# Performance work log

Measured on AMD Instinct MI355X. Metric: run time of the kernel, lower is better.

Reference implementation:

```python
import jax, jax.numpy as jnp
import numpy as np

NUM_QUBITS = 13
NUM_LAYERS = 2


def setup_inputs() -> dict:
    key = jax.random.key(0)
    k1, k2 = jax.random.split(key)
    x = jax.random.normal(k1, (512, 2 ** NUM_QUBITS), dtype=jnp.float32)
    weights = jax.random.normal(k2, (NUM_LAYERS, NUM_QUBITS, 3), dtype=jnp.float32)
    return {"x": x, "weights": weights}


def _rot_matrix(phi, theta, omega):
    # qml.Rot(phi, theta, omega) = RZ(omega) @ RY(theta) @ RZ(phi)
    c = jnp.cos(theta * 0.5).astype(jnp.complex64)
    s = jnp.sin(theta * 0.5).astype(jnp.complex64)
    e_m = jnp.exp((-0.5j) * (phi + omega).astype(jnp.complex64))
    e_p = jnp.exp((0.5j) * (phi + omega).astype(jnp.complex64))
    e_d = jnp.exp((0.5j) * (phi - omega).astype(jnp.complex64))
    e_dc = jnp.exp((-0.5j) * (phi - omega).astype(jnp.complex64))
    row0 = jnp.stack([e_m * c, -e_d * s])
    row1 = jnp.stack([e_dc * s, e_p * c])
    return jnp.stack([row0, row1])  # (2, 2) complex64


def _apply_1q(psi, U, q):
    # psi: (B, 2, 2, ..., 2); contract qubit axis q with 2x2 gate U
    ax = 1 + q
    psi = jnp.moveaxis(psi, ax, -1)
    psi = psi @ U.T
    return jnp.moveaxis(psi, -1, ax)


def _apply_cnot(psi, c, t):
    # X on target where control bit == 1
    s0 = jax.lax.index_in_dim(psi, 0, axis=1 + c, keepdims=True)
    s1 = jax.lax.index_in_dim(psi, 1, axis=1 + c, keepdims=True)
    s1 = jnp.flip(s1, axis=1 + t)
    return jnp.concatenate([s0, s1], axis=1 + c)


def reference(x, weights):
    n = NUM_QUBITS
    B = x.shape[0]
    # AmplitudeEmbedding with normalize=True
    norm = jnp.sqrt(jnp.sum(x * x, axis=1, keepdims=True))
    psi = (x / norm).astype(jnp.complex64).reshape((B,) + (2,) * n)
    # StronglyEntanglingLayers (default ranges r_l = (l % (n-1)) + 1, CNOT imprimitive)
    for l in range(NUM_LAYERS):
        r = (l % (n - 1)) + 1
        for q in range(n):
            U = _rot_matrix(weights[l, q, 0], weights[l, q, 1], weights[l, q, 2])
            psi = _apply_1q(psi, U, q)
        for q in range(n):
            psi = _apply_cnot(psi, q, (q + r) % n)
    # expval(PauliZ(n // 2)) = p(bit=0) - p(bit=1)
    m = n // 2
    probs = jnp.real(psi) ** 2 + jnp.imag(psi) ** 2
    axes = tuple(i for i in range(1, n + 1) if i != 1 + m)
    p = probs.sum(axis=axes)  # (B, 2)
    return p[:, 0] - p[:, 1]
```

## Files before the change

kernel.cpp:

```cpp
#include <hip/hip_runtime.h>
#include <math.h>

#define NQ    13
#define DIM   8192
#define BLOCK 512
#define NGATE 26


__device__ __forceinline__ int SW(int a) { return a ^ (((a >> 7) & 7) << 2); }

struct PCols { int c[NQ]; };
constexpr PCols make_cols(int r) {
    PCols P{};
    for (int b = 0; b < NQ; ++b) {
        int cc = 1 << b;
        for (int cq = 0; cq < NQ; ++cq) {
            const int cb = 12 - cq;
            const int tb = 12 - ((cq + r) % NQ);
            cc ^= ((cc >> cb) & 1) << tb;
        }
        P.c[b] = cc;
    }
    return P;
}
constexpr PCols C1 = make_cols(1);
constexpr int make_rm6() {
    int m = 0;
    for (int b = 0; b < NQ; ++b) m |= ((make_cols(2).c[b] >> 6) & 1) << b;
    return m;
}
constexpr int RM6 = make_rm6();

struct Combos { int k[16]; };
constexpr Combos make_combos() {
    Combos K{};
    for (int j = 0; j < 16; ++j)
        K.k[j] = ((j & 1) ? C1.c[0] : 0) ^ ((j & 2) ? C1.c[1] : 0)
               ^ ((j & 4) ? C1.c[10] : 0) ^ ((j & 8) ? C1.c[11] : 0);
    return K;
}
constexpr Combos KC = make_combos();

constexpr int make_sjw() {
    int wv = 0;
    for (int j = 0; j < 16; ++j) {
        const int jm = (j & 3) | (((j >> 2) & 3) << 10);
        wv |= (__builtin_popcount(jm & RM6) & 1) << j;
    }
    return wv;
}
constexpr int SJW = make_sjw();

__device__ __forceinline__ float2 f2mul(float s, float2 a) {
    return make_float2(s * a.x, s * a.y);
}
__device__ __forceinline__ float2 f2fma(float s, float2 a, float2 b) {
    return make_float2(fmaf(s, a.x, b.x), fmaf(s, a.y, b.y));
}
__device__ __forceinline__ float2 fswap(float2 a) { return make_float2(-a.y, a.x); }

struct G8 { float4 a, b; };
__device__ __forceinline__ G8 ldg8(const float* gm, int gi) {
    G8 g;
    g.a = *(const float4*)&gm[gi * 8];
    g.b = *(const float4*)&gm[gi * 8 + 4];
    return g;
}

template<int P>
__device__ __forceinline__ void rotp(float2* c, const G8 g) {
    #pragma unroll
    for (int m = 0; m < 8; ++m) {
        const int j0 = ((m >> P) << (P + 1)) | (m & ((1 << P) - 1));
        const int j1 = j0 | (1 << P);
        const float2 a0 = c[j0], a1 = c[j1];
        const float2 s0 = fswap(a0), s1 = fswap(a1);
        c[j0] = f2fma(g.a.w, s1, f2fma(g.a.z, a1, f2fma(g.a.y, s0, f2mul(g.a.x, a0))));
        c[j1] = f2fma(g.b.w, s1, f2fma(g.b.z, a1, f2fma(g.b.y, s0, f2mul(g.b.x, a0))));
    }
}

template<int CTRL>
__device__ __forceinline__ float dppx(float v) {
    return __int_as_float(
        __builtin_amdgcn_update_dpp(0, __float_as_int(v), CTRL, 0xf, 0xf, true));
}
template<int CTRL>
__device__ __forceinline__ void rotlane(float2* c, const G8 g, const bool hi) {
    const float Ar = hi ? g.b.z : g.a.x;
    const float Ai = hi ? g.b.w : g.a.y;
    const float Br = hi ? g.b.x : g.a.z;
    const float Bi = hi ? g.b.y : g.a.w;
    #pragma unroll
    for (int j = 0; j < 16; ++j) {
        const float2 p  = make_float2(dppx<CTRL>(c[j].x), dppx<CTRL>(c[j].y));
        const float2 so = fswap(c[j]), sp = fswap(p);
        c[j] = f2fma(Bi, sp, f2fma(Br, p, f2fma(Ai, so, f2mul(Ar, c[j]))));
    }
}

__device__ __forceinline__ void loadgrp(const float* re, const float* im, int a, float2* c) {
    const float4 r = *(const float4*)&re[a];
    const float4 i = *(const float4*)&im[a];
    c[0] = make_float2(r.x, i.x); c[1] = make_float2(r.y, i.y);
    c[2] = make_float2(r.z, i.z); c[3] = make_float2(r.w, i.w);
}
__device__ __forceinline__ void storegrp(float* re, float* im, int a, const float2* c) {
    *(float4*)&re[a] = make_float4(c[0].x, c[1].x, c[2].x, c[3].x);
    *(float4*)&im[a] = make_float4(c[0].y, c[1].y, c[2].y, c[3].y);
}

__global__ __launch_bounds__(BLOCK, 4) void qsim_kernel(
    const float* __restrict__ x,
    const float* __restrict__ w,
    float* __restrict__ out)
{
    __shared__ __align__(16) float re[DIM];
    __shared__ __align__(16) float im[DIM];
    __shared__ __align__(16) float gm[NGATE * 8];
    __shared__ float red_ss[8], red_acc[8];

    const int b = blockIdx.x;
    const int t = threadIdx.x;

    if (t < NGATE) {
        const float phi = w[t * 3 + 0], theta = w[t * 3 + 1], omega = w[t * 3 + 2];
        float co, si;  sincosf(0.5f * theta, &si, &co);
        float sps, cps, sds, cds;
        sincosf(0.5f * (phi + omega), &sps, &cps);
        sincosf(0.5f * (phi - omega), &sds, &cds);
        float* g = &gm[t * 8];
        g[0] =  cps * co;  g[1] = -sps * co;
        g[2] = -cds * si;  g[3] = -sds * si;
        g[4] =  cds * si;  g[5] = -sds * si;
        g[6] =  cps * co;  g[7] =  sps * co;
    }

    const float4* x4 = (const float4*)(x + (size_t)b * DIM);
    float ss = 0.f;
    #pragma unroll
    for (int k = 0; k < 4; ++k) {
        const int m = t + BLOCK * k;
        const int a = SW(4 * m);
        const float4 v = x4[m];
        *(float4*)&re[a] = v;
        ss += v.x * v.x + v.y * v.y + v.z * v.z + v.w * v.w;
    }
    #pragma unroll
    for (int off = 32; off > 0; off >>= 1) ss += __shfl_down(ss, off, 64);
    if ((t & 63) == 0) red_ss[t >> 6] = ss;
    __syncthreads();
    float total = 0.f;
    #pragma unroll
    for (int i = 0; i < 8; ++i) total += red_ss[i];

    float2 c[16];

    const int base2 = (((t >> 2) & 15) << 2) | ((t & 3) << 8) | (((t >> 6) & 7) << 10);
    const int base3 = (((t >> 1) & 255) << 2) | ((t & 1) << 12);

    #pragma unroll
    for (int l = 0; l < 2; ++l) {
        const int G = l * 13;

        if (l == 0) {
            #pragma unroll
            for (int g = 0; g < 4; ++g) {
                const float4 r = *(const float4*)&re[SW((t << 4) | (g << 2))];
                c[4 * g + 0] = make_float2(r.x, 0.f);
                c[4 * g + 1] = make_float2(r.y, 0.f);
                c[4 * g + 2] = make_float2(r.z, 0.f);
                c[4 * g + 3] = make_float2(r.w, 0.f);
            }
        } else {
            #pragma unroll
            for (int g = 0; g < 4; ++g)
                loadgrp(re, im, SW((t << 4) | (g << 2)), &c[4 * g]);
        }
        rotp<0>(c, ldg8(gm, G + 12));
        rotp<1>(c, ldg8(gm, G + 11));
        rotp<2>(c, ldg8(gm, G + 10));
        rotp<3>(c, ldg8(gm, G +  9));
        rotlane<0xB1>(c, ldg8(gm, G + 8), (t & 1) != 0);
        rotlane<0x4E>(c, ldg8(gm, G + 7), (t & 2) != 0);
        #pragma unroll
        for (int g = 0; g < 4; ++g)
            storegrp(re, im, SW((t << 4) | (g << 2)), &c[4 * g]);
        __syncthreads();

        #pragma unroll
        for (int h = 0; h < 4; ++h) loadgrp(re, im, SW(base2 | (h << 6)), &c[4 * h]);
        rotp<2>(c, ldg8(gm, G + 6));
        rotp<3>(c, ldg8(gm, G + 5));
        rotlane<0xB1>(c, ldg8(gm, G + 4), (t & 1) != 0);
        rotlane<0x4E>(c, ldg8(gm, G + 3), (t & 2) != 0);
        #pragma unroll
        for (int h = 0; h < 4; ++h) storegrp(re, im, SW(base2 | (h << 6)), &c[4 * h]);
        __syncthreads();

        #pragma unroll
        for (int h = 0; h < 4; ++h) loadgrp(re, im, SW(base3 | (h << 10)), &c[4 * h]);
        if (l == 0) __syncthreads();
        rotp<2>(c, ldg8(gm, G + 2));
        rotp<3>(c, ldg8(gm, G + 1));
        rotlane<0xB1>(c, ldg8(gm, G + 0), (t & 1) != 0);

        if (l == 0) {
            int mb = 0;
            if (t & 1) mb ^= C1.c[12];
            #pragma unroll
            for (int bb = 0; bb < 8; ++bb)
                if ((t >> (bb + 1)) & 1) mb ^= C1.c[2 + bb];
            #pragma unroll
            for (int j = 0; j < 16; ++j) {
                const int a = SW(mb ^ KC.k[j]);
                re[a] = c[j].x; im[a] = c[j].y;
            }
            __syncthreads();
        }
    }

    const int sbase = __popc(base3 & RM6) & 1;
    float acc = 0.f;
    #pragma unroll
    for (int j = 0; j < 16; ++j) {
        const float p = c[j].x * c[j].x + c[j].y * c[j].y;
        acc += (sbase ^ ((SJW >> j) & 1)) ? -p : p;
    }
    #pragma unroll
    for (int off = 32; off > 0; off >>= 1) acc += __shfl_down(acc, off, 64);
    if ((t & 63) == 0) red_acc[t >> 6] = acc;
    __syncthreads();
    if (t == 0) {
        float tot = 0.f;
        #pragma unroll
        for (int i = 0; i < 8; ++i) tot += red_acc[i];
        out[b] = tot / total;
    }
}

extern "C" void kernel_launch(void* const* d_in, const int* in_sizes, int n_in,
                              void* d_out, int out_size, void* d_ws, size_t ws_size,
                              hipStream_t stream) {
    const float* x = (const float*)d_in[0];
    const float* w = (const float*)d_in[1];
    float* out = (float*)d_out;
    const int B = in_sizes[0] / DIM;
    qsim_kernel<<<B, BLOCK, 0, stream>>>(x, w, out);
}
```

Baseline: 85.02 us.

## Process two batch rows per block to amortize gate loads and barriers

Each block now simulates two state vectors at once, with a separate shared-memory buffer for each, and the grid is halved. Every gate coefficient load, DPP lane exchange setup and __syncthreads is shared by both rows, which adds instruction-level parallelism between independent streams. In exchange the block uses twice the LDS (about 128KB) and roughly twice the registers, so the occupancy bound drops to 2 blocks and the grid has only 256 blocks for 256 CUs. It also assumes the batch size is even.

```diff
diff --git a/kernel.cpp b/kernel.cpp
--- a/kernel.cpp
+++ b/kernel.cpp
@@ -110,15 +110,17 @@
     *(float4*)&im[a] = make_float4(c[0].y, c[1].y, c[2].y, c[3].y);
 }
 
-__global__ __launch_bounds__(BLOCK, 4) void qsim_kernel(
+__global__ __launch_bounds__(BLOCK, 2) void qsim_kernel(
     const float* __restrict__ x,
     const float* __restrict__ w,
     float* __restrict__ out)
 {
-    __shared__ __align__(16) float re[DIM];
-    __shared__ __align__(16) float im[DIM];
+    __shared__ __align__(16) float reA[DIM];
+    __shared__ __align__(16) float imA[DIM];
+    __shared__ __align__(16) float reB[DIM];
+    __shared__ __align__(16) float imB[DIM];
     __shared__ __align__(16) float gm[NGATE * 8];
-    __shared__ float red_ss[8], red_acc[8];
+    __shared__ float red_sA[8], red_sB[8], red_aA[8], red_aB[8];
 
     const int b = blockIdx.x;
     const int t = threadIdx.x;
@@ -136,25 +138,32 @@
         g[6] =  cps * co;  g[7] =  sps * co;
     }
 
-    const float4* x4 = (const float4*)(x + (size_t)b * DIM);
-    float ss = 0.f;
+    const float4* xA4 = (const float4*)(x + (size_t)(2 * b)     * DIM);
+    const float4* xB4 = (const float4*)(x + (size_t)(2 * b + 1) * DIM);
+    float ssA = 0.f, ssB = 0.f;
     #pragma unroll
     for (int k = 0; k < 4; ++k) {
         const int m = t + BLOCK * k;
         const int a = SW(4 * m);
-        const float4 v = x4[m];
-        *(float4*)&re[a] = v;
-        ss += v.x * v.x + v.y * v.y + v.z * v.z + v.w * v.w;
-    }
-    #pragma unroll
-    for (int off = 32; off > 0; off >>= 1) ss += __shfl_down(ss, off, 64);
-    if ((t & 63) == 0) red_ss[t >> 6] = ss;
+        const float4 vA = xA4[m];
+        const float4 vB = xB4[m];
+        *(float4*)&reA[a] = vA;
+        *(float4*)&reB[a] = vB;
+        ssA += vA.x * vA.x + vA.y * vA.y + vA.z * vA.z + vA.w * vA.w;
+        ssB += vB.x * vB.x + vB.y * vB.y + vB.z * vB.z + vB.w * vB.w;
+    }
+    #pragma unroll
+    for (int off = 32; off > 0; off >>= 1) {
+        ssA += __shfl_down(ssA, off, 64);
+        ssB += __shfl_down(ssB, off, 64);
+    }
+    if ((t & 63) == 0) { red_sA[t >> 6] = ssA; red_sB[t >> 6] = ssB; }
     __syncthreads();
-    float total = 0.f;
-    #pragma unroll
-    for (int i = 0; i < 8; ++i) total += red_ss[i];
-
-    float2 c[16];
+    float totalA = 0.f, totalB = 0.f;
+    #pragma unroll
+    for (int i = 0; i < 8; ++i) { totalA += red_sA[i]; totalB += red_sB[i]; }
+
+    float2 cA[16], cB[16];
 
     const int base2 = (((t >> 2) & 15) << 2) | ((t & 3) << 8) | (((t >> 6) & 7) << 10);
     const int base3 = (((t >> 1) & 255) << 2) | ((t & 1) << 12);
@@ -166,44 +175,73 @@
         if (l == 0) {
             #pragma unroll
             for (int g = 0; g < 4; ++g) {
-                const float4 r = *(const float4*)&re[SW((t << 4) | (g << 2))];
-                c[4 * g + 0] = make_float2(r.x, 0.f);
-                c[4 * g + 1] = make_float2(r.y, 0.f);
-                c[4 * g + 2] = make_float2(r.z, 0.f);
-                c[4 * g + 3] = make_float2(r.w, 0.f);
+                const int a = SW((t << 4) | (g << 2));
+                const float4 rA = *(const float4*)&reA[a];
+                const float4 rB = *(const float4*)&reB[a];
+                cA[4 * g + 0] = make_float2(rA.x, 0.f);
+                cA[4 * g + 1] = make_float2(rA.y, 0.f);
+                cA[4 * g + 2] = make_float2(rA.z, 0.f);
+                cA[4 * g + 3] = make_float2(rA.w, 0.f);
+                cB[4 * g + 0] = make_float2(rB.x, 0.f);
+                cB[4 * g + 1] = make_float2(rB.y, 0.f);
+                cB[4 * g + 2] = make_float2(rB.z, 0.f);
+                cB[4 * g + 3] = make_float2(rB.w, 0.f);
             }
         } else {
             #pragma unroll
-            for (int g = 0; g < 4; ++g)
-                loadgrp(re, im, SW((t << 4) | (g << 2)), &c[4 * g]);
-        }
-        rotp<0>(c, ldg8(gm, G + 12));
-        rotp<1>(c, ldg8(gm, G + 11));
-        rotp<2>(c, ldg8(gm, G + 10));
-        rotp<3>(c, ldg8(gm, G +  9));
-        rotlane<0xB1>(c, ldg8(gm, G + 8), (t & 1) != 0);
-        rotlane<0x4E>(c, ldg8(gm, G + 7), (t & 2) != 0);
-        #pragma unroll
-        for (int g = 0; g < 4; ++g)
-            storegrp(re, im, SW((t << 4) | (g << 2)), &c[4 * g]);
+            for (int g = 0; g < 4; ++g) {
+                const int a = SW((t << 4) | (g << 2));
+                loadgrp(reA, imA, a, &cA[4 * g]);
+                loadgrp(reB, imB, a, &cB[4 * g]);
+            }
+        }
+        { const G8 gq = ldg8(gm, G + 12); rotp<0>(cA, gq); rotp<0>(cB, gq); }
+        { const G8 gq = ldg8(gm, G + 11); rotp<1>(cA, gq); rotp<1>(cB, gq); }
+        { const G8 gq = ldg8(gm, G + 10); rotp<2>(cA, gq); rotp<2>(cB, gq); }
+        { const G8 gq = ldg8(gm, G +  9); rotp<3>(cA, gq); rotp<3>(cB, gq); }
+        { const G8 gq = ldg8(gm, G + 8); const bool h = (t & 1) != 0;
+          rotlane<0xB1>(cA, gq, h); rotlane<0xB1>(cB, gq, h); }
+        { const G8 gq = ldg8(gm, G + 7); const bool h = (t & 2) != 0;
+          rotlane<0x4E>(cA, gq, h); rotlane<0x4E>(cB, gq, h); }
+        #pragma unroll
+        for (int g = 0; g < 4; ++g) {
+            const int a = SW((t << 4) | (g << 2));
+            storegrp(reA, imA, a, &cA[4 * g]);
+            storegrp(reB, imB, a, &cB[4 * g]);
+        }
         __syncthreads();
 
         #pragma unroll
-        for (int h = 0; h < 4; ++h) loadgrp(re, im, SW(base2 | (h << 6)), &c[4 * h]);
-        rotp<2>(c, ldg8(gm, G + 6));
-        rotp<3>(c, ldg8(gm, G + 5));
-        rotlane<0xB1>(c, ldg8(gm, G + 4), (t & 1) != 0);
-        rotlane<0x4E>(c, ldg8(gm, G + 3), (t & 2) != 0);
-        #pragma unroll
-        for (int h = 0; h < 4; ++h) storegrp(re, im, SW(base2 | (h << 6)), &c[4 * h]);
+        for (int h = 0; h < 4; ++h) {
+            const int a = SW(base2 | (h << 6));
+            loadgrp(reA, imA, a, &cA[4 * h]);
+            loadgrp(reB, imB, a, &cB[4 * h]);
+        }
+        { const G8 gq = ldg8(gm, G + 6); rotp<2>(cA, gq); rotp<2>(cB, gq); }
+        { const G8 gq = ldg8(gm, G + 5); rotp<3>(cA, gq); rotp<3>(cB, gq); }
+        { const G8 gq = ldg8(gm, G + 4); const bool h = (t & 1) != 0;
+          rotlane<0xB1>(cA, gq, h); rotlane<0xB1>(cB, gq, h); }
+        { const G8 gq = ldg8(gm, G + 3); const bool h = (t & 2) != 0;
+          rotlane<0x4E>(cA, gq, h); rotlane<0x4E>(cB, gq, h); }
+        #pragma unroll
+        for (int h = 0; h < 4; ++h) {
+            const int a = SW(base2 | (h << 6));
+            storegrp(reA, imA, a, &cA[4 * h]);
+            storegrp(reB, imB, a, &cB[4 * h]);
+        }
         __syncthreads();
 
         #pragma unroll
-        for (int h = 0; h < 4; ++h) loadgrp(re, im, SW(base3 | (h << 10)), &c[4 * h]);
+        for (int h = 0; h < 4; ++h) {
+            const int a = SW(base3 | (h << 10));
+            loadgrp(reA, imA, a, &cA[4 * h]);
+            loadgrp(reB, imB, a, &cB[4 * h]);
+        }
         if (l == 0) __syncthreads();
-        rotp<2>(c, ldg8(gm, G + 2));
-        rotp<3>(c, ldg8(gm, G + 1));
-        rotlane<0xB1>(c, ldg8(gm, G + 0), (t & 1) != 0);
+        { const G8 gq = ldg8(gm, G + 2); rotp<2>(cA, gq); rotp<2>(cB, gq); }
+        { const G8 gq = ldg8(gm, G + 1); rotp<3>(cA, gq); rotp<3>(cB, gq); }
+        { const G8 gq = ldg8(gm, G + 0); const bool h = (t & 1) != 0;
+          rotlane<0xB1>(cA, gq, h); rotlane<0xB1>(cB, gq, h); }
 
         if (l == 0) {
             int mb = 0;
@@ -214,28 +252,36 @@
             #pragma unroll
             for (int j = 0; j < 16; ++j) {
                 const int a = SW(mb ^ KC.k[j]);
-                re[a] = c[j].x; im[a] = c[j].y;
+                reA[a] = cA[j].x; imA[a] = cA[j].y;
+                reB[a] = cB[j].x; imB[a] = cB[j].y;
             }
             __syncthreads();
         }
     }
 
     const int sbase = __popc(base3 & RM6) & 1;
-    float acc = 0.f;
+    float accA = 0.f, accB = 0.f;
     #pragma unroll
     for (int j = 0; j < 16; ++j) {
-        const float p = c[j].x * c[j].x + c[j].y * c[j].y;
-        acc += (sbase ^ ((SJW >> j) & 1)) ? -p : p;
-    }
-    #pragma unroll
-    for (int off = 32; off > 0; off >>= 1) acc += __shfl_down(acc, off, 64);
-    if ((t & 63) == 0) red_acc[t >> 6] = acc;
+        const float pA = cA[j].x * cA[j].x + cA[j].y * cA[j].y;
+        const float pB = cB[j].x * cB[j].x + cB[j].y * cB[j].y;
+        const bool neg = (sbase ^ ((SJW >> j) & 1)) != 0;
+        accA += neg ? -pA : pA;
+        accB += neg ? -pB : pB;
+    }
+    #pragma unroll
+    for (int off = 32; off > 0; off >>= 1) {
+        accA += __shfl_down(accA, off, 64);
+        accB += __shfl_down(accB, off, 64);
+    }
+    if ((t & 63) == 0) { red_aA[t >> 6] = accA; red_aB[t >> 6] = accB; }
     __syncthreads();
     if (t == 0) {
-        float tot = 0.f;
-        #pragma unroll
-        for (int i = 0; i < 8; ++i) tot += red_acc[i];
-        out[b] = tot / total;
+        float tA = 0.f, tB = 0.f;
+        #pragma unroll
+        for (int i = 0; i < 8; ++i) { tA += red_aA[i]; tB += red_aB[i]; }
+        out[2 * b]     = tA / totalA;
+        out[2 * b + 1] = tB / totalB;
     }
 }
 
@@ -246,5 +292,5 @@
     const float* w = (const float*)d_in[1];
     float* out = (float*)d_out;
     const int B = in_sizes[0] / DIM;
-    qsim_kernel<<<B, BLOCK, 0, stream>>>(x, w, out);
-}
+    qsim_kernel<<<B / 2, BLOCK, 0, stream>>>(x, w, out);
+}
```

Result: slower. 88.36 us (+3.9%).
